# Optimization experiments

Hardware: AMD Instinct MI355X
Metric: run time of the kernel (lower is better)

The kernel has to match this reference:

```python
import jax, jax.numpy as jnp
import numpy as np

B, N, H = 64, 512, 1024
NH = 8            # attention heads
HD = H // NH      # head dim
STEPS = 24


def setup_inputs() -> dict:
    key = jax.random.key(0)
    ks = jax.random.split(key, 12)
    s = 0.05  # weight scale to keep gates/softmax in a sane range
    return {
        "encoder_outputs": jax.random.normal(ks[0], (B, N, H), dtype=jnp.float32),
        "hidden": jax.random.normal(ks[1], (B, H), dtype=jnp.float32) * s,
        "cell": jax.random.normal(ks[2], (B, H), dtype=jnp.float32) * s,
        "end_node_embed": jax.random.normal(ks[3], (B, H), dtype=jnp.float32),
        "initial_input": jax.random.normal(ks[4], (B, 3 * H), dtype=jnp.float32),
        "max_steps": STEPS,
        # LSTMCell params (torch layout: [4H, in], gate order i,f,g,o)
        "W_ih": jax.random.normal(ks[5], (4 * H, 3 * H), dtype=jnp.float32) * s,
        "b_ih": jnp.zeros((4 * H,), jnp.float32),
        "W_hh": jax.random.normal(ks[6], (4 * H, H), dtype=jnp.float32) * s,
        "b_hh": jnp.zeros((4 * H,), jnp.float32),
        # MultiheadAttention params (torch in_proj [3H,H] = [Wq;Wk;Wv])
        "attn_in_w": jax.random.normal(ks[7], (3 * H, H), dtype=jnp.float32) * s,
        "attn_in_b": jnp.zeros((3 * H,), jnp.float32),
        "attn_out_w": jax.random.normal(ks[8], (H, H), dtype=jnp.float32) * s,
        "attn_out_b": jnp.zeros((H,), jnp.float32),
        # query_transform Linear
        "qt_w": jax.random.normal(ks[9], (H, H), dtype=jnp.float32) * s,
        "qt_b": jnp.zeros((H,), jnp.float32),
    }


def reference(encoder_outputs, hidden, cell, end_node_embed, initial_input,
              max_steps, W_ih, b_ih, W_hh, b_hh,
              attn_in_w, attn_in_b, attn_out_w, attn_out_b, qt_w, qt_b):
    b, n, h = encoder_outputs.shape
    nh, hd = NH, H // NH
    Wq, Wk, Wv = jnp.split(attn_in_w, 3, axis=0)
    bq, bk, bv = jnp.split(attn_in_b, 3)
    S = max_steps
    dt = encoder_outputs.dtype
    buf0 = jnp.zeros((b, S, h), dt)  # preallocated KV cache of decoder hiddens
    neg = jnp.asarray(-1e30, dt)
    scale = 1.0 / jnp.sqrt(jnp.asarray(hd, dt))
    pos = jnp.arange(S)

    def step(carry, t):
        hn, cn, x, buf = carry
        # --- LSTMCell (torch gate order i,f,g,o) ---
        gates = x @ W_ih.T + b_ih + hn @ W_hh.T + b_hh
        i, f, g, o = jnp.split(gates, 4, axis=-1)
        cn = jax.nn.sigmoid(f) * cn + jax.nn.sigmoid(i) * jnp.tanh(g)
        hn = jax.nn.sigmoid(o) * jnp.tanh(cn)
        buf = buf.at[:, t, :].set(hn)
        # --- causal self-attention: q = current hidden, kv = all hiddens <= t ---
        q = (hn @ Wq.T + bq).reshape(b, nh, hd)
        k = (buf @ Wk.T + bk).reshape(b, S, nh, hd)
        v = (buf @ Wv.T + bv).reshape(b, S, nh, hd)
        scores = jnp.einsum('bhd,bshd->bhs', q, k) * scale
        scores = jnp.where((pos > t)[None, None, :], neg, scores)
        attn = jax.nn.softmax(scores, axis=-1)
        ctx = jnp.einsum('bhs,bshd->bhd', attn, v).reshape(b, h)
        attn_out = ctx @ attn_out_w.T + attn_out_b
        # --- pointer scoring ---
        query = (0.5 * (hn + attn_out)) @ qt_w.T + qt_b
        logits = jnp.einsum('bh,bnh->bn', query, encoder_outputs)  # [B,N]
        _, idx = jax.lax.top_k(logits, 3)
        idx = jnp.sort(idx, axis=1)
        top3 = jnp.take_along_axis(encoder_outputs, idx[:, :, None], axis=1)  # [B,3,H]
        x = top3.reshape(b, 3 * h)
        return (hn, cn, x, buf), (logits, idx)

    _, (logits, idx) = jax.lax.scan(
        step, (hidden, cell, initial_input, buf0), jnp.arange(S))
    return logits, idx  # [max_steps,B,N], [max_steps,B,3]
```

## Files before the change

kernel.cpp:

```cpp
#include <hip/hip_runtime.h>
#include <math.h>

#define B_  64
#define N_  512
#define H_  1024
#define NH_ 8
#define HD_ 128
#define S_  24

__global__ __launch_bounds__(256) void wc_pre(
    const float* __restrict__ Wqt, const float* __restrict__ Wout,
    const float* __restrict__ bout, const float* __restrict__ bqt,
    float* __restrict__ W2, float* __restrict__ bc)
{
  __shared__ float As[16][68];
  __shared__ float Bs[16][68];
  const int tid = threadIdx.x;
  const int k0 = (blockIdx.x & 15) * 64;
  const int n0 = (blockIdx.x >> 4) * 64;
  const int tn = tid & 15, tm = tid >> 4;

#pragma unroll
  for (int i = 0; i < 4; ++i) {
    int n = n0 + tm * 4 + i;
    float4 w = *(const float4*)(Wqt + (size_t)n * 1024 + k0 + tn * 4);
    *(float4*)(W2 + (size_t)n * 2048 + k0 + tn * 4) =
        make_float4(0.5f * w.x, 0.5f * w.y, 0.5f * w.z, 0.5f * w.w);
  }

  float acc[4][4];
#pragma unroll
  for (int i = 0; i < 4; ++i)
#pragma unroll
    for (int j = 0; j < 4; ++j) acc[i][j] = 0.f;

  for (int m0 = 0; m0 < 1024; m0 += 16) {
    {
      int nn = tid >> 2, mm = (tid & 3) * 4;
      float4 a = *(const float4*)(Wqt + (size_t)(n0 + nn) * 1024 + m0 + mm);
      As[mm + 0][nn] = a.x; As[mm + 1][nn] = a.y;
      As[mm + 2][nn] = a.z; As[mm + 3][nn] = a.w;
      int mr = tid >> 4, kc = (tid & 15) * 4;
      float4 b = *(const float4*)(Wout + (size_t)(m0 + mr) * 1024 + k0 + kc);
      *(float4*)(&Bs[mr][kc]) = b;
    }
    __syncthreads();
#pragma unroll
    for (int m = 0; m < 16; ++m) {
      float av[4], bv[4];
      *(float4*)av = *(const float4*)(&As[m][tm * 4]);
      *(float4*)bv = *(const float4*)(&Bs[m][tn * 4]);
#pragma unroll
      for (int i = 0; i < 4; ++i)
#pragma unroll
        for (int j = 0; j < 4; ++j)
          acc[i][j] = fmaf(av[i], bv[j], acc[i][j]);
    }
    __syncthreads();
  }
#pragma unroll
  for (int i = 0; i < 4; ++i) {
    int n = n0 + tm * 4 + i;
    *(float4*)(W2 + (size_t)n * 2048 + 1024 + k0 + tn * 4) =
        make_float4(0.5f * acc[i][0], 0.5f * acc[i][1],
                    0.5f * acc[i][2], 0.5f * acc[i][3]);
  }

  {
    int w = tid >> 6, lane = tid & 63;
    int n = blockIdx.x * 4 + w;
    const float* row = Wqt + (size_t)n * 1024;
    float s = 0.f;
#pragma unroll
    for (int c = 0; c < 4; ++c) {
      float4 a = *(const float4*)(row + lane * 16 + c * 4);
      float4 b = *(const float4*)(bout + lane * 16 + c * 4);
      s = fmaf(a.x, b.x, fmaf(a.y, b.y, fmaf(a.z, b.z, fmaf(a.w, b.w, s))));
    }
#pragma unroll
    for (int off = 32; off > 0; off >>= 1) s += __shfl_down(s, off, 64);
    if (lane == 0) bc[n] = 0.5f * s + bqt[n];
  }
}

__device__ __forceinline__ float sigm(float x) { return 1.f / (1.f + expf(-x)); }

__device__ __forceinline__ void ins3(float v, int i,
    float& v0, int& i0, float& v1, int& i1, float& v2, int& i2)
{
  if (v > v0 || (v == v0 && i < i0)) {
    v2 = v1; i2 = i1; v1 = v0; i1 = i0; v0 = v; i0 = i;
  } else if (v > v1 || (v == v1 && i < i1)) {
    v2 = v1; i2 = i1; v1 = v; i1 = i;
  } else if (v > v2 || (v == v2 && i < i2)) {
    v2 = v; i2 = i;
  }
}

__global__ __launch_bounds__(512, 2) void gemm5(
    const float* __restrict__ A0, int ldA0, const float* __restrict__ W0, int ldW0,
    int K0,
    const float* __restrict__ A1, int ldA1, const float* __restrict__ W1, int ldW1,
    const float* __restrict__ enc, const int* __restrict__ idxi, int gather,
    float* __restrict__ P, int N, int KS)
{
  __shared__ float As[16 * 68];
  __shared__ float Bs[16 * 132];
  const int tid = threadIdx.x;
  const int nb = blockIdx.x, sp = blockIdx.y;
  const int ks = sp * KS;

  const float* A; const float* W; int ldA, ldW, koff; int seg0;
  if (ks < K0) { A = A0; W = W0; ldA = ldA0; ldW = ldW0; koff = ks; seg0 = 1; }
  else { A = A1; W = W1; ldA = ldA1; ldW = ldW1; koff = ks - K0; seg0 = 0; }

  const int tn = tid & 31, tm = tid >> 5;
  const int lr = tid >> 2, lc = (tid & 3) * 4;

  float acc[4][4];
#pragma unroll
  for (int i = 0; i < 4; ++i)
#pragma unroll
    for (int j = 0; j < 4; ++j) acc[i][j] = 0.f;

  const float* Wrow = W + (size_t)(nb * 128 + lr) * ldW + koff + lc;
  const float* Arow = nullptr;
  if (tid < 256) {
    if (seg0 && gather) {
      int ei = idxi[lr * 3 + (koff >> 10)];
      Arow = enc + ((size_t)lr * 512 + ei) * 1024 + (koff & 1023) + lc;
    } else {
      Arow = A + (size_t)lr * ldA + koff + lc;
    }
  }

  float4 b4 = *(const float4*)(Wrow);
  float4 a4 = make_float4(0.f, 0.f, 0.f, 0.f);
  if (tid < 256) a4 = *(const float4*)(Arow);

  for (int k0 = 0; k0 < KS; k0 += 16) {
    if (tid < 256) {
      As[(lc + 0) * 68 + lr] = a4.x; As[(lc + 1) * 68 + lr] = a4.y;
      As[(lc + 2) * 68 + lr] = a4.z; As[(lc + 3) * 68 + lr] = a4.w;
    }
    Bs[(lc + 0) * 132 + lr] = b4.x; Bs[(lc + 1) * 132 + lr] = b4.y;
    Bs[(lc + 2) * 132 + lr] = b4.z; Bs[(lc + 3) * 132 + lr] = b4.w;
    __syncthreads();
    if (k0 + 16 < KS) {
      b4 = *(const float4*)(Wrow + k0 + 16);
      if (tid < 256) a4 = *(const float4*)(Arow + k0 + 16);
    }
#pragma unroll
    for (int k = 0; k < 16; ++k) {
      float av[4], bv[4];
      *(float4*)av = *(const float4*)(As + k * 68 + tm * 4);
      *(float4*)bv = *(const float4*)(Bs + k * 132 + tn * 4);
#pragma unroll
      for (int i = 0; i < 4; ++i)
#pragma unroll
        for (int j = 0; j < 4; ++j)
          acc[i][j] = fmaf(av[i], bv[j], acc[i][j]);
    }
    __syncthreads();
  }
  float* Pb = P + (size_t)sp * 64 * N + nb * 128;
#pragma unroll
  for (int i = 0; i < 4; ++i)
    *(float4*)(Pb + (size_t)(tm * 4 + i) * N + tn * 4) =
        make_float4(acc[i][0], acc[i][1], acc[i][2], acc[i][3]);
}

__global__ __launch_bounds__(256) void lstm_red(
    const float* __restrict__ P, const float* __restrict__ b_ih,
    const float* __restrict__ b_hh, const float* __restrict__ c_in,
    float* __restrict__ h_out, float* __restrict__ c_out)
{
  int idx = blockIdx.x * 256 + threadIdx.x;
  int b = idx >> 8, j4 = (idx & 255) * 4;
  float g[4][4];
#pragma unroll
  for (int c = 0; c < 4; ++c) {
    int n = c * 1024 + j4;
    float4 s = *(const float4*)(b_ih + n);
    float4 s2 = *(const float4*)(b_hh + n);
    s.x += s2.x; s.y += s2.y; s.z += s2.z; s.w += s2.w;
#pragma unroll
    for (int sp = 0; sp < 16; ++sp) {
      float4 v = *(const float4*)(P + ((size_t)sp * 64 + b) * 4096 + n);
      s.x += v.x; s.y += v.y; s.z += v.z; s.w += v.w;
    }
    g[c][0] = s.x; g[c][1] = s.y; g[c][2] = s.z; g[c][3] = s.w;
  }
  float4 cp = *(const float4*)(c_in + b * 1024 + j4);
  float cv[4] = {cp.x, cp.y, cp.z, cp.w};
  float4 ho, co;
  float* hp = &ho.x; float* cpn = &co.x;
#pragma unroll
  for (int e = 0; e < 4; ++e) {
    float c = sigm(g[1][e]) * cv[e] + sigm(g[0][e]) * tanhf(g[2][e]);
    cpn[e] = c;
    hp[e] = sigm(g[3][e]) * tanhf(c);
  }
  *(float4*)(c_out + b * 1024 + j4) = co;
  *(float4*)(h_out + b * 1024 + j4) = ho;
}

__global__ __launch_bounds__(128) void attn_fused(
    const float* __restrict__ P, const float* __restrict__ bqkv,
    float* __restrict__ Kc, float* __restrict__ Vc,
    float* __restrict__ ctx, int t)
{
  const float scale = 0.08838834764831845f;
  int bh = blockIdx.x;
  int b = bh >> 3, h = bh & 7;
  int d = threadIdx.x;
  __shared__ float qs[128];
  __shared__ float sc[S_];

  const float* Pb = P + (size_t)b * 3072 + h * 128 + d;
  float qv = bqkv[h * 128 + d];
  float kv = bqkv[1024 + h * 128 + d];
  float vv = bqkv[2048 + h * 128 + d];
#pragma unroll
  for (int sp = 0; sp < 16; ++sp) {
    const float* pp = Pb + (size_t)sp * 64 * 3072;
    qv += pp[0]; kv += pp[1024]; vv += pp[2048];
  }
  float* Kb = Kc + (size_t)(b * NH_ + h) * S_ * HD_;
  float* Vb = Vc + (size_t)(b * NH_ + h) * S_ * HD_;
  Kb[t * 128 + d] = kv;
  Vb[t * 128 + d] = vv;
  qs[d] = qv;
  __syncthreads();

  int wave = d >> 6, lane = d & 63;
  for (int s = wave; s <= t; s += 2) {
    float pr = qs[lane] * Kb[s * 128 + lane] + qs[lane + 64] * Kb[s * 128 + lane + 64];
#pragma unroll
    for (int off = 32; off > 0; off >>= 1) pr += __shfl_down(pr, off, 64);
    if (lane == 0) sc[s] = pr * scale;
  }
  __syncthreads();

  float m = -3.4e38f;
  for (int s = 0; s <= t; ++s) m = fmaxf(m, sc[s]);
  float den = 0.f;
  for (int s = 0; s <= t; ++s) den += expf(sc[s] - m);
  float acc = 0.f;
  for (int s = 0; s <= t; ++s) acc += expf(sc[s] - m) * Vb[s * 128 + d];
  ctx[(size_t)b * 1024 + h * 128 + d] = acc / den;
}

__device__ __forceinline__ float dot16(
    const float4& q0, const float4& q1, const float4& q2, const float4& q3,
    const float4& e0, const float4& e1, const float4& e2, const float4& e3)
{
  float s = 0.f;
  s = fmaf(q0.x, e0.x, s); s = fmaf(q0.y, e0.y, s);
  s = fmaf(q0.z, e0.z, s); s = fmaf(q0.w, e0.w, s);
  s = fmaf(q1.x, e1.x, s); s = fmaf(q1.y, e1.y, s);
  s = fmaf(q1.z, e1.z, s); s = fmaf(q1.w, e1.w, s);
  s = fmaf(q2.x, e2.x, s); s = fmaf(q2.y, e2.y, s);
  s = fmaf(q2.z, e2.z, s); s = fmaf(q2.w, e2.w, s);
  s = fmaf(q3.x, e3.x, s); s = fmaf(q3.y, e3.y, s);
  s = fmaf(q3.z, e3.z, s); s = fmaf(q3.w, e3.w, s);
  return s;
}

__global__ __launch_bounds__(256) void logits4(
    const float* __restrict__ P, const float* __restrict__ bc,
    const float* __restrict__ enc, float* __restrict__ out,
    float* __restrict__ candv, int* __restrict__ candi)
{
  __shared__ float qs[1024];
  __shared__ float cv[12];
  __shared__ int   ci[12];
  const int tid = threadIdx.x;
  const int b = blockIdx.x >> 4, ng = blockIdx.x & 15;

  {
    const int j4 = tid * 4;
    float4 s = *(const float4*)(bc + j4);
#pragma unroll
    for (int sp = 0; sp < 32; ++sp) {
      float4 v = *(const float4*)(P + ((size_t)sp * 64 + b) * 1024 + j4);
      s.x += v.x; s.y += v.y; s.z += v.z; s.w += v.w;
    }
    *(float4*)(qs + j4) = s;
  }
  __syncthreads();

  const int wave = tid >> 6, lane = tid & 63;
  float4 q0 = *(const float4*)(qs + lane * 4);
  float4 q1 = *(const float4*)(qs + 256 + lane * 4);
  float4 q2 = *(const float4*)(qs + 512 + lane * 4);
  float4 q3 = *(const float4*)(qs + 768 + lane * 4);

  const int row0 = ng * 32 + wave * 8;
  const float* eb = enc + ((size_t)b * N_ + row0) * 1024 + lane * 4;
  float* lo = out + (size_t)b * N_ + row0;
  float v0 = -3.4e38f, v1 = -3.4e38f, v2 = -3.4e38f;
  int i0 = 0x7fffffff, i1 = 0x7fffffff, i2 = 0x7fffffff;
  float myout = 0.f;

  float4 A0 = *(const float4*)(eb);
  float4 A1 = *(const float4*)(eb + 256);
  float4 A2 = *(const float4*)(eb + 512);
  float4 A3 = *(const float4*)(eb + 768);
  float4 A4 = *(const float4*)(eb + 1024);
  float4 A5 = *(const float4*)(eb + 1280);
  float4 A6 = *(const float4*)(eb + 1536);
  float4 A7 = *(const float4*)(eb + 1792);

#pragma unroll
  for (int p = 0; p < 4; ++p) {
    const int r = p * 2;
    float4 B0, B1, B2, B3, B4, B5, B6, B7;
    if (p < 3) {
      const float* ea = eb + (size_t)(r + 2) * 1024;
      B0 = *(const float4*)(ea);
      B1 = *(const float4*)(ea + 256);
      B2 = *(const float4*)(ea + 512);
      B3 = *(const float4*)(ea + 768);
      B4 = *(const float4*)(ea + 1024);
      B5 = *(const float4*)(ea + 1280);
      B6 = *(const float4*)(ea + 1536);
      B7 = *(const float4*)(ea + 1792);
    }
    float s0 = dot16(q0, q1, q2, q3, A0, A1, A2, A3);
    float s1 = dot16(q0, q1, q2, q3, A4, A5, A6, A7);
#pragma unroll
    for (int off = 32; off > 0; off >>= 1) {
      s0 += __shfl_xor(s0, off, 64);
      s1 += __shfl_xor(s1, off, 64);
    }
    if (lane == r) myout = s0;
    if (lane == r + 1) myout = s1;
    ins3(s0, row0 + r, v0, i0, v1, i1, v2, i2);
    ins3(s1, row0 + r + 1, v0, i0, v1, i1, v2, i2);
    if (p < 3) {
      A0 = B0; A1 = B1; A2 = B2; A3 = B3;
      A4 = B4; A5 = B5; A6 = B6; A7 = B7;
    }
  }
  if (lane < 8) lo[lane] = myout;
  if (lane == 0) {
    cv[wave * 3 + 0] = v0; ci[wave * 3 + 0] = i0;
    cv[wave * 3 + 1] = v1; ci[wave * 3 + 1] = i1;
    cv[wave * 3 + 2] = v2; ci[wave * 3 + 2] = i2;
  }
  __syncthreads();
  if (tid == 0) {
    float w0 = -3.4e38f, w1 = -3.4e38f, w2 = -3.4e38f;
    int j0 = 0x7fffffff, j1 = 0x7fffffff, j2 = 0x7fffffff;
#pragma unroll
    for (int k = 0; k < 12; ++k)
      ins3(cv[k], ci[k], w0, j0, w1, j1, w2, j2);
    candv[blockIdx.x * 3 + 0] = w0; candi[blockIdx.x * 3 + 0] = j0;
    candv[blockIdx.x * 3 + 1] = w1; candi[blockIdx.x * 3 + 1] = j1;
    candv[blockIdx.x * 3 + 2] = w2; candi[blockIdx.x * 3 + 2] = j2;
  }
}

__global__ __launch_bounds__(64) void top3_merge(
    const float* __restrict__ candv, const int* __restrict__ candi,
    float* __restrict__ idx_out, int* __restrict__ idxi)
{
  int b = threadIdx.x;
  float v0 = -3.4e38f, v1 = -3.4e38f, v2 = -3.4e38f;
  int i0 = 0x7fffffff, i1 = 0x7fffffff, i2 = 0x7fffffff;
  const int base = b * 48;
#pragma unroll
  for (int k = 0; k < 48; ++k)
    ins3(candv[base + k], candi[base + k], v0, i0, v1, i1, v2, i2);
  int a = i0, bb = i1, c = i2, tw;
  if (a > bb) { tw = a; a = bb; bb = tw; }
  if (bb > c) { tw = bb; bb = c; c = tw; }
  if (a > bb) { tw = a; a = bb; bb = tw; }
  idxi[b * 3 + 0] = a; idxi[b * 3 + 1] = bb; idxi[b * 3 + 2] = c;
  idx_out[b * 3 + 0] = (float)a;
  idx_out[b * 3 + 1] = (float)bb;
  idx_out[b * 3 + 2] = (float)c;
}

extern "C" void kernel_launch(void* const* d_in, const int* in_sizes, int n_in,
                              void* d_out, int out_size, void* d_ws, size_t ws_size,
                              hipStream_t stream)
{
  (void)in_sizes; (void)n_in; (void)out_size; (void)ws_size;
  const float* enc   = (const float*)d_in[0];
  const float* h0    = (const float*)d_in[1];
  const float* c0    = (const float*)d_in[2];
  const float* x0    = (const float*)d_in[4];
  const float* W_ih  = (const float*)d_in[6];
  const float* b_ih  = (const float*)d_in[7];
  const float* W_hh  = (const float*)d_in[8];
  const float* b_hh  = (const float*)d_in[9];
  const float* Wqkv  = (const float*)d_in[10];
  const float* bqkv  = (const float*)d_in[11];
  const float* Wout  = (const float*)d_in[12];
  const float* bout  = (const float*)d_in[13];
  const float* Wqt   = (const float*)d_in[14];
  const float* bqt   = (const float*)d_in[15];

  float* ws    = (float*)d_ws;
  float* P     = ws;
  float* W2    = P + 16 * 64 * 4096;
  float* bc    = W2 + 1024 * 2048;
  float* hbuf  = bc + 1024;
  float* cbuf  = hbuf + 64 * 1024;
  float* ctx   = cbuf + 64 * 1024;
  float* Kc    = ctx + 64 * 1024;
  float* Vc    = Kc + 64 * NH_ * S_ * HD_;
  float* candv = Vc + 64 * NH_ * S_ * HD_;
  int*   candi = (int*)(candv + 1024 * 3);
  int*   idxi  = candi + 1024 * 3;

  float* logits_out = (float*)d_out;
  float* idx_out    = logits_out + (size_t)S_ * B_ * N_;

  wc_pre<<<dim3(256), dim3(256), 0, stream>>>(Wqt, Wout, bout, bqt, W2, bc);

  for (int t = 0; t < S_; ++t) {
    const float* xin   = (t == 0) ? x0 : nullptr;
    const float* hprev = (t == 0) ? h0 : hbuf;
    const float* cprev = (t == 0) ? c0 : cbuf;

    gemm5<<<dim3(32, 16), dim3(512), 0, stream>>>(
        xin, 3072, W_ih, 3072, 3072,
        hprev, 1024, W_hh, 1024,
        enc, idxi, t > 0, P, 4096, 256);
    lstm_red<<<dim3(64), dim3(256), 0, stream>>>(P, b_ih, b_hh, cprev, hbuf, cbuf);

    gemm5<<<dim3(24, 16), dim3(512), 0, stream>>>(
        hbuf, 1024, Wqkv, 1024, 1024,
        hbuf, 1024, Wqkv, 1024,
        enc, idxi, 0, P, 3072, 64);
    attn_fused<<<dim3(512), dim3(128), 0, stream>>>(P, bqkv, Kc, Vc, ctx, t);

    gemm5<<<dim3(8, 32), dim3(512), 0, stream>>>(
        hbuf, 1024, W2, 2048, 1024,
        ctx, 1024, W2 + 1024, 2048,
        enc, idxi, 0, P, 1024, 64);

    logits4<<<dim3(1024), dim3(256), 0, stream>>>(
        P, bc, enc, logits_out + (size_t)t * B_ * N_, candv, candi);
    top3_merge<<<dim3(1), dim3(64), 0, stream>>>(
        candv, candi, idx_out + (size_t)t * B_ * 3, idxi);
  }
}
```

Before: 3.811 ms.

## Prepack GEMM weights into tile-contiguous layout and halve split-K count

Adds a one-time wpack kernel that rearranges W_ih/W_hh, Wqkv and the fused W2 into per-block, per-k-step contiguous tiles, so each GEMM block streams its weight tile with fully coalesced float4 loads instead of strided row reads. The split-K factor is halved (larger KS per block) for all three GEMMs, so the reduction kernels sum half as many partials and P shrinks. The trade-off is fewer blocks per launch (lower parallelism), extra workspace and packing kernels run on every call.

```diff
diff --git a/kernel.cpp b/kernel.cpp
--- a/kernel.cpp
+++ b/kernel.cpp
@@ -83,6 +83,24 @@
   }
 }
 
+__global__ __launch_bounds__(512) void wpack(
+    const float* __restrict__ src, int ldSrc, int NB, int KS, int spBase,
+    float* __restrict__ dst)
+{
+  const int tid = threadIdx.x;
+  const int nb = blockIdx.x, spl = blockIdx.y;
+  const int tpr = KS >> 2;
+  const int rpp = 512 / tpr;
+  float* dt = dst + ((size_t)(spBase + spl) * NB + nb) * (size_t)(128 * KS);
+  const float* sb = src + (size_t)nb * 128 * ldSrc + (size_t)spl * KS;
+  const int rloc = tid / tpr, c4 = (tid % tpr) * 4;
+  for (int p = 0; p < 128 / rpp; ++p) {
+    int row = p * rpp + rloc;
+    float4 v = *(const float4*)(sb + (size_t)row * ldSrc + c4);
+    *(float4*)(dt + (c4 >> 4) * 2048 + row * 16 + (c4 & 12)) = v;
+  }
+}
+
 __device__ __forceinline__ float sigm(float x) { return 1.f / (1.f + expf(-x)); }
 
 __device__ __forceinline__ void ins3(float v, int i,
@@ -97,10 +115,10 @@
   }
 }
 
-__global__ __launch_bounds__(512, 2) void gemm5(
-    const float* __restrict__ A0, int ldA0, const float* __restrict__ W0, int ldW0,
-    int K0,
-    const float* __restrict__ A1, int ldA1, const float* __restrict__ W1, int ldW1,
+__global__ __launch_bounds__(512, 2) void gemmP(
+    const float* __restrict__ A0, int ldA0, int K0,
+    const float* __restrict__ A1, int ldA1,
+    const float* __restrict__ Wp, int NB,
     const float* __restrict__ enc, const int* __restrict__ idxi, int gather,
     float* __restrict__ P, int N, int KS)
 {
@@ -110,10 +128,6 @@
   const int nb = blockIdx.x, sp = blockIdx.y;
   const int ks = sp * KS;
 
-  const float* A; const float* W; int ldA, ldW, koff; int seg0;
-  if (ks < K0) { A = A0; W = W0; ldA = ldA0; ldW = ldW0; koff = ks; seg0 = 1; }
-  else { A = A1; W = W1; ldA = ldA1; ldW = ldW1; koff = ks - K0; seg0 = 0; }
-
   const int tn = tid & 31, tm = tid >> 5;
   const int lr = tid >> 2, lc = (tid & 3) * 4;
 
@@ -123,18 +137,22 @@
 #pragma unroll
     for (int j = 0; j < 4; ++j) acc[i][j] = 0.f;
 
-  const float* Wrow = W + (size_t)(nb * 128 + lr) * ldW + koff + lc;
+  const float* Wt = Wp + ((size_t)sp * NB + nb) * (size_t)(128 * KS);
   const float* Arow = nullptr;
   if (tid < 256) {
-    if (seg0 && gather) {
-      int ei = idxi[lr * 3 + (koff >> 10)];
-      Arow = enc + ((size_t)lr * 512 + ei) * 1024 + (koff & 1023) + lc;
+    if (ks < K0) {
+      if (gather) {
+        int ei = idxi[lr * 3 + (ks >> 10)];
+        Arow = enc + ((size_t)lr * 512 + ei) * 1024 + (ks & 1023) + lc;
+      } else {
+        Arow = A0 + (size_t)lr * ldA0 + ks + lc;
+      }
     } else {
-      Arow = A + (size_t)lr * ldA + koff + lc;
-    }
-  }
-
-  float4 b4 = *(const float4*)(Wrow);
+      Arow = A1 + (size_t)lr * ldA1 + (ks - K0) + lc;
+    }
+  }
+
+  float4 b4 = *(const float4*)(Wt + tid * 4);
   float4 a4 = make_float4(0.f, 0.f, 0.f, 0.f);
   if (tid < 256) a4 = *(const float4*)(Arow);
 
@@ -147,7 +165,7 @@
     Bs[(lc + 2) * 132 + lr] = b4.z; Bs[(lc + 3) * 132 + lr] = b4.w;
     __syncthreads();
     if (k0 + 16 < KS) {
-      b4 = *(const float4*)(Wrow + k0 + 16);
+      b4 = *(const float4*)(Wt + (k0 + 16) * 128 + tid * 4);
       if (tid < 256) a4 = *(const float4*)(Arow + k0 + 16);
     }
 #pragma unroll
@@ -185,7 +203,7 @@
     float4 s2 = *(const float4*)(b_hh + n);
     s.x += s2.x; s.y += s2.y; s.z += s2.z; s.w += s2.w;
 #pragma unroll
-    for (int sp = 0; sp < 16; ++sp) {
+    for (int sp = 0; sp < 8; ++sp) {
       float4 v = *(const float4*)(P + ((size_t)sp * 64 + b) * 4096 + n);
       s.x += v.x; s.y += v.y; s.z += v.z; s.w += v.w;
     }
@@ -222,7 +240,7 @@
   float kv = bqkv[1024 + h * 128 + d];
   float vv = bqkv[2048 + h * 128 + d];
 #pragma unroll
-  for (int sp = 0; sp < 16; ++sp) {
+  for (int sp = 0; sp < 8; ++sp) {
     const float* pp = Pb + (size_t)sp * 64 * 3072;
     qv += pp[0]; kv += pp[1024]; vv += pp[2048];
   }
@@ -282,7 +300,7 @@
     const int j4 = tid * 4;
     float4 s = *(const float4*)(bc + j4);
 #pragma unroll
-    for (int sp = 0; sp < 32; ++sp) {
+    for (int sp = 0; sp < 16; ++sp) {
       float4 v = *(const float4*)(P + ((size_t)sp * 64 + b) * 1024 + j4);
       s.x += v.x; s.y += v.y; s.z += v.z; s.w += v.w;
     }
@@ -405,7 +423,7 @@
 
   float* ws    = (float*)d_ws;
   float* P     = ws;
-  float* W2    = P + 16 * 64 * 4096;
+  float* W2    = P + 8 * 64 * 4096;
   float* bc    = W2 + 1024 * 2048;
   float* hbuf  = bc + 1024;
   float* cbuf  = hbuf + 64 * 1024;
@@ -415,33 +433,37 @@
   float* candv = Vc + 64 * NH_ * S_ * HD_;
   int*   candi = (int*)(candv + 1024 * 3);
   int*   idxi  = candi + 1024 * 3;
+  float* Wg_p  = (float*)(idxi + 192 + 64);
+  float* Wq_p  = Wg_p + (size_t)8 * 32 * 128 * 512;
+  float* W2_p  = Wq_p + (size_t)8 * 24 * 128 * 128;
 
   float* logits_out = (float*)d_out;
   float* idx_out    = logits_out + (size_t)S_ * B_ * N_;
 
   wc_pre<<<dim3(256), dim3(256), 0, stream>>>(Wqt, Wout, bout, bqt, W2, bc);
+  wpack<<<dim3(32, 6), dim3(512), 0, stream>>>(W_ih, 3072, 32, 512, 0, Wg_p);
+  wpack<<<dim3(32, 2), dim3(512), 0, stream>>>(W_hh, 1024, 32, 512, 6, Wg_p);
+  wpack<<<dim3(24, 8), dim3(512), 0, stream>>>(Wqkv, 1024, 24, 128, 0, Wq_p);
+  wpack<<<dim3(8, 16), dim3(512), 0, stream>>>(W2, 2048, 8, 128, 0, W2_p);
 
   for (int t = 0; t < S_; ++t) {
     const float* xin   = (t == 0) ? x0 : nullptr;
     const float* hprev = (t == 0) ? h0 : hbuf;
     const float* cprev = (t == 0) ? c0 : cbuf;
 
-    gemm5<<<dim3(32, 16), dim3(512), 0, stream>>>(
-        xin, 3072, W_ih, 3072, 3072,
-        hprev, 1024, W_hh, 1024,
-        enc, idxi, t > 0, P, 4096, 256);
+    gemmP<<<dim3(32, 8), dim3(512), 0, stream>>>(
+        xin, 3072, 3072, hprev, 1024,
+        Wg_p, 32, enc, idxi, t > 0, P, 4096, 512);
     lstm_red<<<dim3(64), dim3(256), 0, stream>>>(P, b_ih, b_hh, cprev, hbuf, cbuf);
 
-    gemm5<<<dim3(24, 16), dim3(512), 0, stream>>>(
-        hbuf, 1024, Wqkv, 1024, 1024,
-        hbuf, 1024, Wqkv, 1024,
-        enc, idxi, 0, P, 3072, 64);
+    gemmP<<<dim3(24, 8), dim3(512), 0, stream>>>(
+        hbuf, 1024, 1024, hbuf, 1024,
+        Wq_p, 24, enc, idxi, 0, P, 3072, 128);
     attn_fused<<<dim3(512), dim3(128), 0, stream>>>(P, bqkv, Kc, Vc, ctx, t);
 
-    gemm5<<<dim3(8, 32), dim3(512), 0, stream>>>(
-        hbuf, 1024, W2, 2048, 1024,
-        ctx, 1024, W2 + 1024, 2048,
-        enc, idxi, 0, P, 1024, 64);
+    gemmP<<<dim3(8, 16), dim3(512), 0, stream>>>(
+        hbuf, 1024, 1024, ctx, 1024,
+        W2_p, 8, enc, idxi, 0, P, 1024, 128);
 
     logits4<<<dim3(1024), dim3(256), 0, stream>>>(
         P, bc, enc, logits_out + (size_t)t * B_ * N_, candv, candi);
```

After: 4.008 ms. 1.05x slower.
